# Kernel optimization log

Measured on AMD Instinct MI355X. Metric: run time of the kernel, lower is better.

## Reference

```python
import jax, jax.numpy as jnp
import numpy as np

N_NODES = 100000
N_EDGES = 3200000
N_FEATS = 512
HIDDEN = 256
N_CLASSES = 64
K_STEPS = 10
ALPHA = 0.1


def setup_inputs() -> dict:
    key = jax.random.key(0)
    k1, k2, k3, k4 = jax.random.split(key, 4)
    x = jax.random.normal(k1, (N_NODES, N_FEATS), dtype=jnp.float32)
    edge_index = jax.random.randint(k2, (2, N_EDGES), 0, N_NODES, dtype=jnp.int64)
    W1 = jax.random.normal(k3, (N_FEATS, HIDDEN), dtype=jnp.float32) * (1.0 / np.sqrt(N_FEATS))
    b1 = jnp.zeros((HIDDEN,), dtype=jnp.float32)
    W2 = jax.random.normal(k4, (HIDDEN, N_CLASSES), dtype=jnp.float32) * (1.0 / np.sqrt(HIDDEN))
    b2 = jnp.zeros((N_CLASSES,), dtype=jnp.float32)
    return {"x": x, "edge_index": edge_index, "W1": W1, "b1": b1, "W2": W2, "b2": b2}


def reference(x, edge_index, W1, b1, W2, b2):
    # MLP (dropout is identity in eval mode)
    h = jax.nn.relu(x @ W1 + b1)            # [N, hidden]
    h = h @ W2 + b2                          # [N, C]

    # gcn_norm with self-loops: A_hat = D^{-1/2} (A + I) D^{-1/2}
    loop = jnp.arange(N_NODES, dtype=edge_index.dtype)
    src = jnp.concatenate([edge_index[0], loop])  # message source
    dst = jnp.concatenate([edge_index[1], loop])  # aggregation target
    ones = jnp.ones_like(dst, dtype=h.dtype)
    deg = jax.ops.segment_sum(ones, dst, num_segments=N_NODES)
    dinv = jnp.where(deg > 0, jax.lax.rsqrt(jnp.maximum(deg, 1.0)), 0.0)
    norm = dinv[src] * dinv[dst]             # [E+N]

    # APPNP: h_{t+1} = (1-alpha) * A_hat h_t + alpha * h_0
    h0 = h
    def step(hc, _):
        msg = norm[:, None] * hc[src]                       # gather + scale
        agg = jax.ops.segment_sum(msg, dst, num_segments=N_NODES)  # scatter-add
        return (1.0 - ALPHA) * agg + ALPHA * h0, None
    h, _ = jax.lax.scan(step, h, None, length=K_STEPS)

    return jax.nn.log_softmax(h, axis=1)
```

## Files before the change

kernel.cpp:

```cpp
#include <hip/hip_runtime.h>
#include <math.h>

#define NN 100000
#define NE 3200000
#define NF 512
#define NH 256
#define NC 64
#define KSTEPS 10
#define NB 391
#define CAP 96
#define NPH 8
#define FBP 1024

typedef _Float16 half8 __attribute__((ext_vector_type(8)));
typedef float f32x4 __attribute__((ext_vector_type(4)));


__global__ __launch_bounds__(256) void init_k(int* cnt, _Float16* y0, _Float16* yA, _Float16* yB) {
  int i = blockIdx.x * 256 + threadIdx.x;
  if (i < NN) cnt[i] = 0;
  if (blockIdx.x == 0) {
    int t = threadIdx.x;
    if (t < 64)       y0[(size_t)NN * NC + t] = (_Float16)0.f;
    else if (t < 128) yA[(size_t)NN * NC + (t - 64)] = (_Float16)0.f;
    else if (t < 192) yB[(size_t)NN * NC + (t - 128)] = (_Float16)0.f;
  }
}


__global__ __launch_bounds__(256) void fill_k(const int* __restrict__ dstI, const int* __restrict__ srcI,
                                              int* __restrict__ cnt, int* __restrict__ slots) {
  int ph = blockIdx.x / FBP;
  int bi = blockIdx.x - ph * FBP;
  int lo = ph * (NN / NPH);
  int hi = lo + (NN / NPH);
  for (int e = bi * 256 + threadIdx.x; e < NE; e += FBP * 256) {
    int d = dstI[e];
    if (d >= lo && d < hi) {
      int pos = atomicAdd(&cnt[d], 1);
      if (pos < CAP) slots[(size_t)d * CAP + pos] = srcI[e];
    }
  }
}

__global__ __launch_bounds__(256) void pad_k(const int* __restrict__ cnt, int* __restrict__ slots) {
  int d = blockIdx.x * 256 + threadIdx.x;
  if (d >= NN) return;
  int c = cnt[d];
  int e = (c + 15) & ~15;
  for (int p = c; p < e; ++p) slots[(size_t)d * CAP + p] = NN;
}

__global__ __launch_bounds__(256) void dinv_k(const int* __restrict__ cnt, float* dinv, float* dsqrt, float* amul) {
  int i = blockIdx.x * 256 + threadIdx.x;
  if (i < NN) {
    float d = (float)(cnt[i] + 1);
    dinv[i]  = rsqrtf(d);
    dsqrt[i] = sqrtf(d);
    amul[i]  = 0.9f / d;
  }
}


__global__ __launch_bounds__(256) void cvtW1T_k(const float* __restrict__ W1, _Float16* __restrict__ W1T) {
  int t = blockIdx.x * 256 + threadIdx.x;
  int n = t >> 9, k = t & 511;
  W1T[t] = (_Float16)W1[k * NH + n];
}

__global__ __launch_bounds__(256) void cvtW2T_k(const float* __restrict__ W2, _Float16* __restrict__ W2T) {
  int t = blockIdx.x * 256 + threadIdx.x;
  int n = t >> 8, k = t & 255;
  W2T[t] = (_Float16)W2[k * NC + n];
}


__global__ __launch_bounds__(256) void mlp_k(const float* __restrict__ x, const _Float16* __restrict__ W1T,
                                             const float* __restrict__ b1, const _Float16* __restrict__ W2T,
                                             const float* __restrict__ b2, const float* __restrict__ dinv,
                                             _Float16* __restrict__ y0, _Float16* __restrict__ c0) {
  __shared__ _Float16 smem[16896];
  _Float16* As = smem;
  _Float16* Bs = smem + 64 * 40;
  _Float16* Hs = smem;

  const int t    = threadIdx.x;
  const int wave = t >> 6;
  const int lane = t & 63;
  const int l15  = lane & 15;
  const int q    = lane >> 4;
  const int m0   = blockIdx.x * 64;

  f32x4 acc[4][4] = {};

  for (int kk = 0; kk < NF; kk += 32) {
    __syncthreads();
    {
      int row = t >> 2;
      int kq  = (t & 3) << 3;
      int gr  = m0 + row;
      float4 v0 = make_float4(0.f, 0.f, 0.f, 0.f), v1 = v0;
      if (gr < NN) {
        const float* xp = &x[(size_t)gr * NF + kk + kq];
        v0 = *(const float4*)xp;
        v1 = *(const float4*)(xp + 4);
      }
      half8 hv;
      hv[0] = (_Float16)v0.x; hv[1] = (_Float16)v0.y; hv[2] = (_Float16)v0.z; hv[3] = (_Float16)v0.w;
      hv[4] = (_Float16)v1.x; hv[5] = (_Float16)v1.y; hv[6] = (_Float16)v1.z; hv[7] = (_Float16)v1.w;
      *(half8*)&As[row * 40 + kq] = hv;
    }
    #pragma unroll
    for (int i = 0; i < 4; ++i) {
      int idx = t + (i << 8);
      int n   = idx >> 2;
      int kq  = (idx & 3) << 3;
      *(half8*)&Bs[n * 40 + kq] = *(const half8*)&W1T[(size_t)n * NF + kk + kq];
    }
    __syncthreads();
    half8 af[4], bf[4];
    #pragma unroll
    for (int mi = 0; mi < 4; ++mi) af[mi] = *(half8*)&As[(mi * 16 + l15) * 40 + q * 8];
    #pragma unroll
    for (int ni = 0; ni < 4; ++ni) bf[ni] = *(half8*)&Bs[(wave * 64 + ni * 16 + l15) * 40 + q * 8];
    #pragma unroll
    for (int mi = 0; mi < 4; ++mi)
      #pragma unroll
      for (int ni = 0; ni < 4; ++ni)
        acc[mi][ni] = __builtin_amdgcn_mfma_f32_16x16x32_f16(af[mi], bf[ni], acc[mi][ni], 0, 0, 0);
  }
  __syncthreads();

  #pragma unroll
  for (int mi = 0; mi < 4; ++mi) {
    #pragma unroll
    for (int ni = 0; ni < 4; ++ni) {
      int ch = wave * 64 + ni * 16 + l15;
      float bb = b1[ch];
      #pragma unroll
      for (int r = 0; r < 4; ++r) {
        int m = mi * 16 + q * 4 + r;
        float v = acc[mi][ni][r] + bb;
        Hs[m * 264 + ch] = (_Float16)(v > 0.f ? v : 0.f);
      }
    }
  }
  __syncthreads();

  f32x4 acc2[4] = {};
  for (int kt = 0; kt < 8; ++kt) {
    half8 bf2 = *(const half8*)&W2T[(size_t)(wave * 16 + l15) * NH + kt * 32 + q * 8];
    #pragma unroll
    for (int mi = 0; mi < 4; ++mi) {
      half8 af2 = *(half8*)&Hs[(mi * 16 + l15) * 264 + kt * 32 + q * 8];
      acc2[mi] = __builtin_amdgcn_mfma_f32_16x16x32_f16(af2, bf2, acc2[mi], 0, 0, 0);
    }
  }
  int c = wave * 16 + l15;
  float bb2 = b2[c];
  #pragma unroll
  for (int mi = 0; mi < 4; ++mi)
    #pragma unroll
    for (int r = 0; r < 4; ++r) {
      int m = m0 + mi * 16 + q * 4 + r;
      if (m < NN) {
        float hv = acc2[mi][r] + bb2;
        float dv = dinv[m];
        y0[(size_t)m * NC + c] = (_Float16)(dv * hv);
        c0[(size_t)m * NC + c] = (_Float16)(0.1f * dv * hv);
      }
    }
}


__global__ __launch_bounds__(256) void appnp_k(const _Float16* __restrict__ y_in, const _Float16* __restrict__ c0,
                                               _Float16* __restrict__ y_out,
                                               const int* __restrict__ cnt, const int* __restrict__ slots,
                                               const float* __restrict__ amul) {
  int lane = threadIdx.x & 63;
  int node = blockIdx.x * 4 + (threadIdx.x >> 6);
  node = __builtin_amdgcn_readfirstlane(node);
  int pcnt = (cnt[node] + 15) & ~15;
  const int* row = slots + (size_t)node * CAP;
  float a0 = (float)y_in[(size_t)node * NC + lane];
  float a1 = 0.f, a2 = 0.f, a3 = 0.f;
  for (int e = 0; e < pcnt; e += 16) {
    int sj[16];
    #pragma unroll
    for (int j = 0; j < 16; ++j) sj[j] = row[e + j];
    float v[16];
    #pragma unroll
    for (int j = 0; j < 16; ++j) v[j] = (float)y_in[(size_t)sj[j] * NC + lane];
    #pragma unroll
    for (int j = 0; j < 16; j += 4) {
      a0 += v[j]; a1 += v[j + 1]; a2 += v[j + 2]; a3 += v[j + 3];
    }
  }
  size_t o = (size_t)node * NC + lane;
  y_out[o] = (_Float16)(amul[node] * ((a0 + a1) + (a2 + a3)) + (float)c0[o]);
}


__global__ __launch_bounds__(256) void lsm_k(const _Float16* __restrict__ y, const float* __restrict__ dsqrt,
                                             float* __restrict__ out) {
  int lane = threadIdx.x & 63;
  int node = blockIdx.x * 4 + (threadIdx.x >> 6);
  node = __builtin_amdgcn_readfirstlane(node);
  float v = (float)y[(size_t)node * NC + lane] * dsqrt[node];
  float m = v;
  #pragma unroll
  for (int off = 32; off > 0; off >>= 1) m = fmaxf(m, __shfl_xor(m, off, 64));
  float e = expf(v - m);
  float s = e;
  #pragma unroll
  for (int off = 32; off > 0; off >>= 1) s += __shfl_xor(s, off, 64);
  out[(size_t)node * NC + lane] = (v - m) - logf(s);
}


extern "C" void kernel_launch(void* const* d_in, const int* in_sizes, int n_in,
                              void* d_out, int out_size, void* d_ws, size_t ws_size,
                              hipStream_t stream) {
  (void)in_sizes; (void)n_in; (void)out_size; (void)ws_size;
  const float* x  = (const float*)d_in[0];
  const int*   ei = (const int*)d_in[1];
  const float* W1 = (const float*)d_in[2];
  const float* b1 = (const float*)d_in[3];
  const float* W2 = (const float*)d_in[4];
  const float* b2 = (const float*)d_in[5];
  float* out = (float*)d_out;

  const int* srcI = ei;
  const int* dstI = ei + NE;

  char* p = (char*)d_ws;
  auto carve = [&](size_t bytes) -> void* {
    void* q = (void*)p;
    p += (bytes + 255) & ~(size_t)255;
    return q;
  };
  _Float16* y0   = (_Float16*)carve((size_t)(NN + 1) * NC * 2);
  _Float16* yA   = (_Float16*)carve((size_t)(NN + 1) * NC * 2);
  _Float16* yB   = (_Float16*)carve((size_t)(NN + 1) * NC * 2);
  _Float16* c0   = (_Float16*)carve((size_t)NN * NC * 2);
  _Float16* W1T  = (_Float16*)carve((size_t)NH * NF * 2);
  _Float16* W2T  = (_Float16*)carve((size_t)NC * NH * 2);
  float* dinv    = (float*)carve((size_t)NN * 4);
  float* dsqrt   = (float*)carve((size_t)NN * 4);
  float* amul    = (float*)carve((size_t)NN * 4);
  int*   cnt     = (int*)carve((size_t)NN * 4);
  int*   slots   = (int*)carve((size_t)NN * CAP * 4);

  init_k   <<<NB, 256, 0, stream>>>(cnt, y0, yA, yB);
  fill_k   <<<NPH * FBP, 256, 0, stream>>>(dstI, srcI, cnt, slots);
  pad_k    <<<NB, 256, 0, stream>>>(cnt, slots);
  dinv_k   <<<NB, 256, 0, stream>>>(cnt, dinv, dsqrt, amul);
  cvtW1T_k <<<(NH * NF) / 256, 256, 0, stream>>>(W1, W1T);
  cvtW2T_k <<<(NC * NH) / 256, 256, 0, stream>>>(W2, W2T);
  mlp_k    <<<(NN + 63) / 64, 256, 0, stream>>>(x, W1T, b1, W2T, b2, dinv, y0, c0);

  const _Float16* yin = y0;
  _Float16* bufs[2] = { yA, yB };
  for (int it = 0; it < KSTEPS; ++it) {
    _Float16* yo = bufs[it & 1];
    appnp_k<<<NN / 4, 256, 0, stream>>>(yin, c0, yo, cnt, slots, amul);
    yin = yo;
  }
  lsm_k<<<NN / 4, 256, 0, stream>>>(yin, dsqrt, out);
}
```

Measured before the change: 1.073 ms.

## Vectorize APPNP gather with 4-wide fp16 loads and split edges across quarter-waves

Each lane now loads four fp16 features (8 bytes) per neighbor instead of one. The wave is split into four 16-lane groups that handle different edges at the same time, and a cross-lane shuffle reduction combines their partial sums. Accumulation moves from fp32 to packed fp16, and the write-back becomes a vector store done by one quarter-wave. The aim is fewer memory instructions and better use of each gathered row. The cost is reduced accumulation precision and an extra shuffle reduction.

```diff
diff --git a/kernel.cpp b/kernel.cpp
--- a/kernel.cpp
+++ b/kernel.cpp
@@ -13,6 +13,7 @@
 #define FBP 1024
 
 typedef _Float16 half8 __attribute__((ext_vector_type(8)));
+typedef _Float16 h4v  __attribute__((ext_vector_type(4)));
 typedef float f32x4 __attribute__((ext_vector_type(4)));
 
 
@@ -177,27 +178,44 @@
                                                _Float16* __restrict__ y_out,
                                                const int* __restrict__ cnt, const int* __restrict__ slots,
                                                const float* __restrict__ amul) {
-  int lane = threadIdx.x & 63;
+  const int lane = threadIdx.x & 63;
+  const int qw   = lane >> 4;
+  const int fq   = lane & 15;
   int node = blockIdx.x * 4 + (threadIdx.x >> 6);
   node = __builtin_amdgcn_readfirstlane(node);
-  int pcnt = (cnt[node] + 15) & ~15;
+  const int pcnt = (cnt[node] + 15) & ~15;
   const int* row = slots + (size_t)node * CAP;
-  float a0 = (float)y_in[(size_t)node * NC + lane];
-  float a1 = 0.f, a2 = 0.f, a3 = 0.f;
+  const char* yb = (const char*)y_in;
+  const unsigned foff = (unsigned)fq * 8u;
+
+  h4v acc = { (_Float16)0.f, (_Float16)0.f, (_Float16)0.f, (_Float16)0.f };
   for (int e = 0; e < pcnt; e += 16) {
-    int sj[16];
-    #pragma unroll
-    for (int j = 0; j < 16; ++j) sj[j] = row[e + j];
-    float v[16];
-    #pragma unroll
-    for (int j = 0; j < 16; ++j) v[j] = (float)y_in[(size_t)sj[j] * NC + lane];
-    #pragma unroll
-    for (int j = 0; j < 16; j += 4) {
-      a0 += v[j]; a1 += v[j + 1]; a2 += v[j + 2]; a3 += v[j + 3];
-    }
-  }
-  size_t o = (size_t)node * NC + lane;
-  y_out[o] = (_Float16)(amul[node] * ((a0 + a1) + (a2 + a3)) + (float)c0[o]);
+    #pragma unroll
+    for (int j = 0; j < 4; ++j) {
+      int idx = row[e + j * 4 + qw];
+      unsigned off = (unsigned)idx * 128u + foff;
+      acc += *(const h4v*)(yb + off);
+    }
+  }
+
+  int2 ai = *(int2*)&acc;
+  int2 o1; o1.x = __shfl_xor(ai.x, 16, 64); o1.y = __shfl_xor(ai.y, 16, 64);
+  acc += *(h4v*)&o1;
+  ai = *(int2*)&acc;
+  int2 o2; o2.x = __shfl_xor(ai.x, 32, 64); o2.y = __shfl_xor(ai.y, 32, 64);
+  acc += *(h4v*)&o2;
+
+  if (qw == 0) {
+    size_t rowb = (size_t)node * 128 + foff;
+    h4v self = *(const h4v*)((const char*)y_in + rowb);
+    h4v cc   = *(const h4v*)((const char*)c0   + rowb);
+    float am = amul[node];
+    h4v r;
+    #pragma unroll
+    for (int i = 0; i < 4; ++i)
+      r[i] = (_Float16)(am * ((float)acc[i] + (float)self[i]) + (float)cc[i]);
+    *(h4v*)((char*)y_out + rowb) = r;
+  }
 }
 
 
```

After: 1.066 ms. No clear change (-0.7%).
